# Optimization experiments

Measured on AMD Instinct MI355X. Metric: run time of the kernel, lower is better.

The kernel has to match this reference:

```python
import jax, jax.numpy as jnp
import numpy as np

B, U, I, H = 4096, 6, 1024, 512
IK, IV, K = 64, 400, 4
CH, CK, CV = 4, 32, 512
NS = 4


def setup_inputs() -> dict:
    key = jax.random.key(0)
    ks = jax.random.split(key, 14)
    s = 0.02
    return dict(
        x=jax.random.normal(ks[0], (B, 1, I), jnp.float32),
        hs=jax.random.normal(ks[1], (B, U, H), jnp.float32),
        Wk=jax.random.normal(ks[2], (I, IK), jnp.float32) * s,
        bk=jnp.zeros((IK,), jnp.float32),
        Wv=jax.random.normal(ks[3], (I, IV), jnp.float32) * s,
        bv=jnp.zeros((IV,), jnp.float32),
        Wq=jax.random.normal(ks[4], (U, H, IK), jnp.float32) * s,
        Wq_=jax.random.normal(ks[5], (U, H, CH * CK), jnp.float32) * s,
        Wk_=jax.random.normal(ks[6], (U, H, CH * CK), jnp.float32) * s,
        Wv_=jax.random.normal(ks[7], (U, H, CH * CV), jnp.float32) * s,
        Wo_=jax.random.normal(ks[8], (U, CH * CV, CV), jnp.float32) * s,
        sw=jax.nn.softmax(jax.random.normal(ks[9], (U, NS), jnp.float32), axis=-1),
        gru_wx=jax.random.normal(ks[10], (NS, IV, 3 * H), jnp.float32) * s,
        gru_wh=jax.random.normal(ks[11], (NS, H, 3 * H), jnp.float32) * s,
    )


def reference(x, hs, Wk, bk, Wv, bv, Wq, Wq_, Wk_, Wv_, Wo_, sw, gru_wx, gru_wh):
    b = x.shape[0]
    # append null input along token dim -> (B, 2, I)
    x2 = jnp.concatenate([x, jnp.zeros_like(x)], axis=1)
    # input attention (num_input_heads = 1)
    k_l = x2 @ Wk + bk                                   # (B,2,IK)
    v_l = x2 @ Wv + bv                                   # (B,2,IV)
    q_l = jnp.einsum('buh,uhd->bud', hs, Wq)             # (B,U,IK)
    scores = jnp.einsum('bud,btd->but', q_l, k_l) / np.sqrt(IK).astype(np.float32)
    # top-k gating on the non-null score
    not_null = scores[:, :, 0]                           # (B,U)
    _, idx = jax.lax.top_k(not_null, K)
    mask = jnp.zeros((b, U), x.dtype).at[jnp.arange(b)[:, None], idx].set(1.0)
    probs = jax.nn.softmax(scores, axis=-1)              # dropout off (eval)
    inputs = jnp.einsum('but,btv->buv', probs, v_l) * mask[:, :, None]  # (B,U,IV)
    # shared-schema GroupGRU: per-unit weights = schema mixture
    Wx = jnp.einsum('us,sio->uio', sw, gru_wx)           # (U,IV,3H)
    Wh = jnp.einsum('us,sho->uho', sw, gru_wh)           # (U,H,3H)
    gx = jnp.einsum('bui,uio->buo', inputs, Wx)
    gh = jnp.einsum('buh,uho->buo', hs, Wh)
    xr, xz, xn = jnp.split(gx, 3, axis=-1)
    hr, hz, hn = jnp.split(gh, 3, axis=-1)
    r = jax.nn.sigmoid(xr + hr)
    z = jax.nn.sigmoid(xz + hz)
    n = jnp.tanh(xn + r * hn)
    hy = n + z * (hs - n)                                # (B,U,H)
    # blocked_grad is identity in forward
    h_b = hy
    # communication attention (4 heads)
    q = jnp.einsum('buh,uho->buo', h_b, Wq_).reshape(b, U, CH, CK).transpose(0, 2, 1, 3)
    kk = jnp.einsum('buh,uho->buo', h_b, Wk_).reshape(b, U, CH, CK).transpose(0, 2, 1, 3)
    v = jnp.einsum('buh,uho->buo', h_b, Wv_).reshape(b, U, CH, CV).transpose(0, 2, 1, 3)
    att = jnp.einsum('bhqd,bhkd->bhqk', q, kk) / np.sqrt(CK).astype(np.float32)
    ap = jax.nn.softmax(att, axis=-1) * mask[:, None, :, None]  # mask query units
    ctx = jnp.einsum('bhqk,bhkd->bhqd', ap, v)           # (B,CH,U,CV)
    ctx = ctx.transpose(0, 2, 1, 3).reshape(b, U, CH * CV)
    ctx = jnp.einsum('buh,uho->buo', ctx, Wo_) + h_b     # (B,U,H)
    m = mask[:, :, None]
    hs_new = m * ctx + (1.0 - m) * hs
    return hs_new
```

## Files before the change

kernel.cpp:

```cpp
#include <hip/hip_runtime.h>
#include <cstddef>
#include <cstdint>


typedef unsigned short u16;
typedef __bf16 bf16x8 __attribute__((ext_vector_type(8)));
typedef float f32x4 __attribute__((ext_vector_type(4)));
typedef u16 u16x4 __attribute__((ext_vector_type(4)));

#define DEVFN static __device__ __forceinline__

DEVFN float ldin(const void* p, size_t i, int f) {
  return f ? (float)reinterpret_cast<const __bf16*>(p)[i]
           : reinterpret_cast<const float*>(p)[i];
}
DEVFN float bf2f(const u16* p, size_t i) {
  return (float)reinterpret_cast<const __bf16*>(p)[i];
}
DEVFN void f2bf(u16* p, size_t i, float v) {
  reinterpret_cast<__bf16*>(p)[i] = (__bf16)v;
}
DEVFN u16 bfbits(float v) {
  __bf16 b = (__bf16)v;
  return *reinterpret_cast<u16*>(&b);
}

constexpr size_t OFF_FLAG = 0;
constexpr size_t OFF_MASK = 256;
constexpr size_t OFF_WVT  = 98560;
constexpr size_t OFF_WQKT = 917760;
constexpr size_t OFF_WVT_ = 2490624;
constexpr size_t OFF_WOT  = 15073536;
constexpr size_t OFF_WXCT = 27656448;
constexpr size_t OFF_WHCT = 35029248;
constexpr size_t OFF_HY   = 44466432;
constexpr size_t ARENA    = 72777984;
constexpr size_t A_INP    = ARENA;
constexpr size_t A_PK     = ARENA;
constexpr size_t A_PQ     = ARENA + 4194304;
constexpr size_t A_P1     = 92438784;
constexpr size_t A_KL     = A_P1;
constexpr size_t A_QL     = 93487360;
constexpr size_t A_VL     = 99778816;

__global__ void rim_detect(const void* sw, int* flagp) {
  if (threadIdx.x == 0) {
    float s = 0.f;
    for (int i = 0; i < 24; i++)
      s += (float)reinterpret_cast<const __bf16*>(sw)[i];
    flagp[0] = (s > 5.5f && s < 6.5f) ? 1 : 0;
  }
}

__global__ __launch_bounds__(256)
void rim_sgemm32(const void* __restrict__ A_, long lda, long Az,
                 const void* __restrict__ W_, long Wz,
                 float* __restrict__ P, int KC,
                 const int* __restrict__ flagp)
{
  const int f = flagp[0];
  __shared__ float As[32 * 33];
  __shared__ float Ws[32 * 68];
  const int t = threadIdx.x;
  const int m0 = blockIdx.x * 32, kc = blockIdx.y, z = blockIdx.z;
  const int Z = gridDim.z;
  const int kb = kc * KC;
  const int tx = t & 15, ty = t >> 4;

  f32x4 acc[2];
#pragma unroll
  for (int i = 0; i < 2; i++)
#pragma unroll
    for (int j = 0; j < 4; j++) acc[i][j] = 0.f;

  for (int k0 = kb; k0 < kb + KC; k0 += 32) {
#pragma unroll
    for (int j = 0; j < 4; j++) {
      int idx = t + j * 256;
      int row = idx >> 5, kk = idx & 31;
      As[row * 33 + kk] =
          ldin(A_, (size_t)(m0 + row) * lda + (size_t)z * Az + k0 + kk, f);
    }
#pragma unroll
    for (int j = 0; j < 8; j++) {
      int idx = t + j * 256;
      int kk = idx >> 6, n = idx & 63;
      Ws[kk * 68 + n] = ldin(W_, (size_t)z * Wz + (size_t)(k0 + kk) * 64 + n, f);
    }
    __syncthreads();
#pragma unroll 8
    for (int kk = 0; kk < 32; kk++) {
      f32x4 wv = *reinterpret_cast<const f32x4*>(&Ws[kk * 68 + tx * 4]);
#pragma unroll
      for (int i = 0; i < 2; i++) {
        float a = As[(ty * 2 + i) * 33 + kk];
#pragma unroll
        for (int j = 0; j < 4; j++) acc[i][j] += a * wv[j];
      }
    }
    __syncthreads();
  }
  float* Pb = P + ((size_t)kc * Z + z) * (4096 * 64);
#pragma unroll
  for (int i = 0; i < 2; i++)
    *reinterpret_cast<f32x4*>(&Pb[(size_t)(m0 + ty * 2 + i) * 64 + tx * 4]) = acc[i];
}

__global__ void rim_sreduce(const float* __restrict__ P, int NK, int Z,
                            float* __restrict__ C, long ldc, long Cz,
                            const void* __restrict__ bias,
                            const int* __restrict__ flagp, long total)
{
  const int f = flagp[0];
  long idx = (long)blockIdx.x * 256 + threadIdx.x;
  if (idx >= total) return;
  long z = idx / (4096 * 64);
  long r = idx - z * (4096 * 64);
  long m = r >> 6;
  int n = (int)(r & 63);
  float s = bias ? ldin(bias, n, f) : 0.f;
  for (int kc = 0; kc < NK; kc++)
    s += P[((size_t)kc * Z + z) * (4096 * 64) + r];
  C[(size_t)m * ldc + (size_t)z * Cz + n] = s;
}

constexpr int LP = 40;
template<int EPI, int ADT>
__global__ __launch_bounds__(256)
void rim_gemm(const void* __restrict__ A_, long A0, long lda, long Az,
              const u16* __restrict__ B_, long Bz,
              void* __restrict__ C_, long C0, long ldc, long Cz,
              int M, int N, int K,
              const void* __restrict__ bias,
              const u16* __restrict__ hyp,
              const float* __restrict__ maskp,
              const void* __restrict__ hsp,
              const int* __restrict__ flagp)
{
  __shared__ __align__(16) __bf16 As[128 * LP];
  __shared__ __align__(16) __bf16 Bs[128 * LP];
  const int f = flagp[0];
  const int t = threadIdx.x;
  const int m0 = blockIdx.x * 128, n0 = blockIdx.y * 128, z = blockIdx.z;
  const __bf16* Bb = reinterpret_cast<const __bf16*>(B_) + (size_t)z * Bz;
  const int lane = t & 63, w = t >> 6;
  const int wm = (w & 1) * 64, wn = (w >> 1) * 64;
  const int lr = lane & 15, lk = (lane >> 4) * 8;

  f32x4 acc[4][4];
#pragma unroll
  for (int i = 0; i < 4; i++)
#pragma unroll
    for (int j = 0; j < 4; j++)
#pragma unroll
      for (int r = 0; r < 4; r++) acc[i][j][r] = 0.f;

  const int r0 = t >> 2;
  const int kc0 = (t & 3) << 3;

  for (int k0 = 0; k0 < K; k0 += 32) {
#pragma unroll
    for (int it = 0; it < 2; it++) {
      int row = r0 + it * 64;
      int gk = k0 + kc0;
      bf16x8 av, bv8;
#pragma unroll
      for (int q = 0; q < 8; q++) { av[q] = (__bf16)0.f; bv8[q] = (__bf16)0.f; }
      int gm = m0 + row;
      if (gm < M && gk < K) {
        if constexpr (ADT == 0) {
          av = *reinterpret_cast<const bf16x8*>(
              reinterpret_cast<const __bf16*>(A_) + (size_t)A0 + (size_t)z * Az +
              (size_t)gm * lda + gk);
        } else {
          size_t idx = (size_t)A0 + (size_t)z * Az + (size_t)gm * lda + gk;
          if (f) {
            av = *reinterpret_cast<const bf16x8*>(
                reinterpret_cast<const __bf16*>(A_) + idx);
          } else {
            const f32x4* fp = reinterpret_cast<const f32x4*>(
                reinterpret_cast<const float*>(A_) + idx);
            f32x4 lo = fp[0], hi = fp[1];
#pragma unroll
            for (int q = 0; q < 4; q++) {
              av[q] = (__bf16)lo[q]; av[q + 4] = (__bf16)hi[q];
            }
          }
        }
      }
      int gn = n0 + row;
      if (gn < N && gk < K)
        bv8 = *reinterpret_cast<const bf16x8*>(Bb + (size_t)gn * (size_t)K + gk);
      *reinterpret_cast<bf16x8*>(&As[row * LP + kc0]) = av;
      *reinterpret_cast<bf16x8*>(&Bs[row * LP + kc0]) = bv8;
    }
    __syncthreads();
    bf16x8 af[4], bg[4];
#pragma unroll
    for (int i = 0; i < 4; i++)
      af[i] = *reinterpret_cast<const bf16x8*>(&As[(wm + i * 16 + lr) * LP + lk]);
#pragma unroll
    for (int j = 0; j < 4; j++)
      bg[j] = *reinterpret_cast<const bf16x8*>(&Bs[(wn + j * 16 + lr) * LP + lk]);
#pragma unroll
    for (int i = 0; i < 4; i++)
#pragma unroll
      for (int j = 0; j < 4; j++)
        acc[i][j] = __builtin_amdgcn_mfma_f32_16x16x32_bf16(af[i], bg[j], acc[i][j], 0, 0, 0);
    __syncthreads();
  }

  const int rq = (lane >> 4) * 4;
  const int cq = lane & 15;
#pragma unroll
  for (int i = 0; i < 4; i++) {
#pragma unroll
    for (int j = 0; j < 4; j++) {
      int cg = n0 + wn + j * 16 + cq;
      if (cg >= N) continue;
#pragma unroll
      for (int r = 0; r < 4; r++) {
        int rg = m0 + wm + i * 16 + rq + r;
        if (rg >= M) continue;
        float v = acc[i][j][r];
        size_t cidx = (size_t)rg * ldc + (size_t)z * Cz + cg;
        if constexpr (EPI == 2) {
          f2bf((u16*)C_, C0 + cidx, v + ldin(bias, cg, f));
        } else if constexpr (EPI == 3) {
          f2bf((u16*)C_, C0 + cidx, v);
        } else {
          float mk = maskp[(size_t)rg * 6 + z];
          if (mk > 0.5f) {
            float o = v + bf2f(hyp, cidx);
            if (f) f2bf((u16*)C_, C0 + cidx, o);
            else   reinterpret_cast<float*>(C_)[C0 + cidx] = o;
          } else {
            if (f) reinterpret_cast<u16*>(C_)[C0 + cidx] =
                       reinterpret_cast<const u16*>(hsp)[C0 + cidx];
            else   reinterpret_cast<float*>(C_)[C0 + cidx] =
                       reinterpret_cast<const float*>(hsp)[C0 + cidx];
          }
        }
      }
    }
  }
}

__global__ __launch_bounds__(256)
void rim_transpose(const void* __restrict__ in, u16* __restrict__ out,
                   int N, int K, long in_z, long out_z,
                   const int* __restrict__ flagp)
{
  const int f = flagp[0];
  __shared__ float tile[32][33];
  int z = blockIdx.z;
  int k0 = blockIdx.x * 32, n0 = blockIdx.y * 32;
  int c = threadIdx.x & 31, r = threadIdx.x >> 5;
  for (int rr = r; rr < 32; rr += 8) {
    int k = k0 + rr, n = n0 + c;
    tile[rr][c] = (k < K && n < N)
        ? ldin(in, (size_t)z * in_z + (size_t)k * N + n, f) : 0.f;
  }
  __syncthreads();
  for (int rr = r; rr < 32; rr += 8) {
    int n = n0 + rr, k = k0 + c;
    if (n < N && k < K)
      f2bf(out, (size_t)z * out_z + (size_t)n * K + k, tile[c][rr]);
  }
}

__global__ __launch_bounds__(256)
void rim_gruw(const void* __restrict__ sw, const void* __restrict__ gw,
              u16* __restrict__ out, int IVH, const int* __restrict__ flagp)
{
  const int f = flagp[0];
  __shared__ float lds[64 * 17];
  int u = blockIdx.z;
  int i0 = blockIdx.x * 16, o0 = blockIdx.y * 64;
  int t = threadIdx.x;
  float s0 = ldin(sw, u * 4 + 0, f), s1 = ldin(sw, u * 4 + 1, f);
  float s2 = ldin(sw, u * 4 + 2, f), s3 = ldin(sw, u * 4 + 3, f);
  int oo = t & 63, iq = t >> 6;
  size_t pl = (size_t)IVH * 1536;
#pragma unroll
  for (int r = 0; r < 4; r++) {
    int ii = iq * 4 + r;
    size_t base = (size_t)(i0 + ii) * 1536 + o0 + oo;
    float acc = s0 * ldin(gw, base, f) + s1 * ldin(gw, pl + base, f) +
                s2 * ldin(gw, 2 * pl + base, f) + s3 * ldin(gw, 3 * pl + base, f);
    lds[oo * 17 + ii] = acc;
  }
  __syncthreads();
  int ow = t >> 2, iw = (t & 3) * 4;
  u16x4 pk;
#pragma unroll
  for (int j = 0; j < 4; j++) pk[j] = bfbits(lds[ow * 17 + iw + j]);
  *reinterpret_cast<u16x4*>(out + ((size_t)u * 1536 + o0 + ow) * IVH + i0 + iw) = pk;
}

__global__ __launch_bounds__(256)
void rim_scores(const float* __restrict__ q_l, const float* __restrict__ k_l0,
                const void* __restrict__ bk, const u16* __restrict__ v_l0,
                const void* __restrict__ bv, float* __restrict__ maskf,
                u16* __restrict__ inputs, const int* __restrict__ flagp)
{
  const int f = flagp[0];
  int b = blockIdx.x;
  int t = threadIdx.x;
  int lane = t & 63;
  __shared__ float s0[6], s1[6], sm[6], sp[6];
  if (t < 64) {
    float kv = k_l0[(size_t)b * 64 + lane];
    for (int u = 0; u < 6; u++) {
      float p = q_l[((size_t)b * 6 + u) * 64 + lane] * kv;
      for (int off = 32; off; off >>= 1) p += __shfl_down(p, off);
      if (lane == 0) s0[u] = p * 0.125f;
    }
  } else if (t < 128) {
    float kv = ldin(bk, lane, f);
    for (int u = 0; u < 6; u++) {
      float p = q_l[((size_t)b * 6 + u) * 64 + lane] * kv;
      for (int off = 32; off; off >>= 1) p += __shfl_down(p, off);
      if (lane == 0) s1[u] = p * 0.125f;
    }
  }
  __syncthreads();
  if (t == 0) {
    for (int u = 0; u < 6; u++) {
      int cnt = 0;
      for (int u2 = 0; u2 < 6; u2++)
        if (s0[u2] > s0[u] || (s0[u2] == s0[u] && u2 < u)) cnt++;
      float mk = (cnt < 4) ? 1.0f : 0.0f;
      sm[u] = mk;
      maskf[(size_t)b * 6 + u] = mk;
      sp[u] = 1.0f / (1.0f + expf(s1[u] - s0[u]));
    }
  }
  __syncthreads();
  for (int idx = t; idx < 2400; idx += 256) {
    int u = idx / 400, j = idx % 400;
    float val = sm[u] * (sp[u] * bf2f(v_l0, (size_t)b * 400 + j) +
                         (1.0f - sp[u]) * ldin(bv, j, f));
    f2bf(inputs, ((size_t)b * 6 + u) * 400 + j, val);
  }
}

__global__ void rim_gru(const u16* __restrict__ Ggx, const u16* __restrict__ Ggh,
                        const void* __restrict__ hs, long R0,
                        u16* __restrict__ hy, long total,
                        const int* __restrict__ flagp)
{
  const int f = flagp[0];
  long idx = (long)blockIdx.x * 256 + threadIdx.x;
  if (idx >= total) return;
  long bu = idx >> 9;
  int h = idx & 511;
  size_t gb = (size_t)bu * 1536 + h;
  float xr = bf2f(Ggx, gb), xz = bf2f(Ggx, gb + 512), xn = bf2f(Ggx, gb + 1024);
  float hr = bf2f(Ggh, gb), hz = bf2f(Ggh, gb + 512), hn = bf2f(Ggh, gb + 1024);
  float r = 1.f / (1.f + expf(-(xr + hr)));
  float zz = 1.f / (1.f + expf(-(xz + hz)));
  float n = tanhf(xn + r * hn);
  float hv = ldin(hs, R0 + idx, f);
  f2bf(hy, idx, n + zz * (hv - n));
}

__global__ __launch_bounds__(256)
void rim_attn(const u16* __restrict__ qk, const float* __restrict__ maskp,
              const u16* __restrict__ v, u16* __restrict__ ctx)
{
  int bl = blockIdx.x;
  int t = threadIdx.x;
  __shared__ float qs[1536];
  __shared__ float aps[144];
  __shared__ __align__(16) u16 vs[12288];
  for (int idx = t; idx < 1536; idx += 256)
    qs[idx] = bf2f(qk, (size_t)bl * 1536 + idx);
  for (int idx = t; idx < 1536; idx += 256)
    *reinterpret_cast<bf16x8*>(&vs[idx * 8]) =
        *reinterpret_cast<const bf16x8*>(
            reinterpret_cast<const __bf16*>(v) + (size_t)bl * 12288 + idx * 8);
  __syncthreads();
  if (t < 144) {
    int h = t / 36, r6 = t % 36, uq = r6 / 6, uk = r6 % 6;
    float s = 0.f;
#pragma unroll
    for (int d = 0; d < 32; d++)
      s += qs[uq * 256 + h * 32 + d] * qs[uk * 256 + 128 + h * 32 + d];
    aps[t] = s * 0.17677669529663687f;
  }
  __syncthreads();
  if (t < 24) {
    int h = t / 6, uq = t % 6;
    float* row = &aps[h * 36 + uq * 6];
    float mx = row[0];
    for (int k = 1; k < 6; k++) mx = fmaxf(mx, row[k]);
    float e[6], sum = 0.f;
    for (int k = 0; k < 6; k++) { e[k] = expf(row[k] - mx); sum += e[k]; }
    float mk = maskp[(size_t)bl * 6 + uq] / sum;
    for (int k = 0; k < 6; k++) row[k] = e[k] * mk;
  }
  __syncthreads();
  for (int idx = t; idx < 12288; idx += 256) {
    int uq = idx >> 11, g = idx & 2047, h = g >> 9;
    const float* ar = &aps[h * 36 + uq * 6];
    float acc = 0.f;
#pragma unroll
    for (int k = 0; k < 6; k++) acc += ar[k] * bf2f(vs, k * 2048 + g);
    f2bf(ctx, ((size_t)bl * 6 + uq) * 2048 + g, acc);
  }
}

extern "C" void kernel_launch(void* const* d_in, const int* in_sizes, int n_in,
                              void* d_out, int out_size, void* d_ws, size_t ws_size,
                              hipStream_t stream)
{
  (void)in_sizes; (void)n_in; (void)out_size;
  const void* x   = d_in[0];
  const void* hs  = d_in[1];
  const void* Wk  = d_in[2];
  const void* bk  = d_in[3];
  const void* Wv  = d_in[4];
  const void* bv  = d_in[5];
  const void* Wq  = d_in[6];
  const void* Wq_ = d_in[7];
  const void* Wk_ = d_in[8];
  const void* Wv_ = d_in[9];
  const void* Wo_ = d_in[10];
  const void* sw  = d_in[11];
  const void* gwx = d_in[12];
  const void* gwh = d_in[13];
  char* ws = (char*)d_ws;

  int*   flagp = (int*)(ws + OFF_FLAG);
  float* maskf = (float*)(ws + OFF_MASK);
  u16* WvT   = (u16*)(ws + OFF_WVT);
  u16* WqkT  = (u16*)(ws + OFF_WQKT);
  u16* WvT_  = (u16*)(ws + OFF_WVT_);
  u16* WoT   = (u16*)(ws + OFF_WOT);
  u16* WxcT  = (u16*)(ws + OFF_WXCT);
  u16* WhcT  = (u16*)(ws + OFF_WHCT);
  u16* hy    = (u16*)(ws + OFF_HY);
  u16* inputs = (u16*)(ws + A_INP);
  float* PK   = (float*)(ws + A_PK);
  float* PQ   = (float*)(ws + A_PQ);
  float* k_l0 = (float*)(ws + A_KL);
  float* q_l  = (float*)(ws + A_QL);
  u16* v_l0   = (u16*)(ws + A_VL);

  int R2 = 256, R3 = 256;
  {
    const int cand[5] = {4096, 2048, 1024, 512, 256};
    for (int i = 0; i < 5; i++)
      if (A_P1 + (size_t)cand[i] * 36864 <= ws_size) { R2 = cand[i]; break; }
    for (int i = 0; i < 5; i++)
      if (ARENA + (size_t)cand[i] * 52224 <= ws_size) { R3 = cand[i]; break; }
  }

  rim_detect<<<dim3(1), dim3(64), 0, stream>>>(sw, flagp);

  auto T = [&](const void* in, u16* outp, int N, int K, long iz, long oz, int Z) {
    dim3 g((K + 31) / 32, (N + 31) / 32, Z);
    rim_transpose<<<g, dim3(256), 0, stream>>>(in, outp, N, K, iz, oz, flagp);
  };
  T(Wv, WvT, 400, 1024, 0, 0, 1);
  T(Wq_, WqkT, 128, 512, 65536, 131072, 6);
  T(Wk_, WqkT + 65536, 128, 512, 65536, 131072, 6);
  T(Wv_, WvT_, 2048, 512, 1048576, 1048576, 6);
  T(Wo_, WoT, 512, 2048, 1048576, 1048576, 6);
  rim_gruw<<<dim3(25, 24, 6), dim3(256), 0, stream>>>(sw, gwx, WxcT, 400, flagp);
  rim_gruw<<<dim3(32, 24, 6), dim3(256), 0, stream>>>(sw, gwh, WhcT, 512, flagp);

  auto G = [&](int epi, int adt, const void* A, long A0, long lda, long Az,
               const u16* B, long Bz, void* C, long C0, long ldc, long Cz,
               int M, int N, int K, int Z,
               const void* bias, const u16* hyp, const float* mp, const void* hsp) {
    dim3 g((M + 127) / 128, (N + 127) / 128, Z), blk(256);
    if (epi == 2 && adt == 1)
      rim_gemm<2, 1><<<g, blk, 0, stream>>>(A, A0, lda, Az, B, Bz, C, C0, ldc, Cz, M, N, K, bias, hyp, mp, hsp, flagp);
    else if (epi == 3 && adt == 1)
      rim_gemm<3, 1><<<g, blk, 0, stream>>>(A, A0, lda, Az, B, Bz, C, C0, ldc, Cz, M, N, K, bias, hyp, mp, hsp, flagp);
    else if (epi == 3 && adt == 0)
      rim_gemm<3, 0><<<g, blk, 0, stream>>>(A, A0, lda, Az, B, Bz, C, C0, ldc, Cz, M, N, K, bias, hyp, mp, hsp, flagp);
    else
      rim_gemm<4, 0><<<g, blk, 0, stream>>>(A, A0, lda, Az, B, Bz, C, C0, ldc, Cz, M, N, K, bias, hyp, mp, hsp, flagp);
  };

  rim_sgemm32<<<dim3(128, 4, 1), dim3(256), 0, stream>>>(
      x, 1024, 0, Wk, 0, PK, 256, flagp);
  rim_sgemm32<<<dim3(128, 2, 6), dim3(256), 0, stream>>>(
      hs, 3072, 512, Wq, 32768, PQ, 256, flagp);
  rim_sreduce<<<dim3(1024), dim3(256), 0, stream>>>(
      PK, 4, 1, k_l0, 64, 0, bk, flagp, 4096L * 64);
  rim_sreduce<<<dim3(6144), dim3(256), 0, stream>>>(
      PQ, 2, 6, q_l, 384, 64, nullptr, flagp, 6L * 4096 * 64);
  G(2, 1, x, 0, 1024, 0, WvT, 0, v_l0, 0, 400, 0, 4096, 400, 1024, 1,
    bv, nullptr, nullptr, nullptr);
  rim_scores<<<dim3(4096), dim3(256), 0, stream>>>(q_l, k_l0, bk, v_l0, bv,
                                                   maskf, inputs, flagp);

  u16* Ggx = (u16*)(ws + A_P1);
  u16* Ggh = (u16*)(ws + A_P1 + (size_t)R2 * 18432);
  for (int r0 = 0; r0 < 4096; r0 += R2) {
    G(3, 1, hs, (long)r0 * 3072, 3072, 512, WhcT, 786432, Ggh, 0, 9216, 1536,
      R2, 1536, 512, 6, nullptr, nullptr, nullptr, nullptr);
    G(3, 0, inputs, (long)r0 * 2400, 2400, 400, WxcT, 614400, Ggx, 0, 9216, 1536,
      R2, 1536, 400, 6, nullptr, nullptr, nullptr, nullptr);
    long total = (long)R2 * 3072;
    rim_gru<<<dim3((unsigned)(total / 256)), dim3(256), 0, stream>>>(
        Ggx, Ggh, hs, (long)r0 * 3072, hy + (size_t)r0 * 3072, total, flagp);
  }

  u16* qk_c  = (u16*)(ws + ARENA);
  u16* v_c   = (u16*)(ws + ARENA + (size_t)R3 * 3072);
  u16* ctx_c = (u16*)(ws + ARENA + (size_t)R3 * 3072 + (size_t)R3 * 24576);
  for (int r0 = 0; r0 < 4096; r0 += R3) {
    G(3, 0, hy, (long)r0 * 3072, 3072, 512, WqkT, 131072, qk_c, 0, 1536, 256,
      R3, 256, 512, 6, nullptr, nullptr, nullptr, nullptr);
    G(3, 0, hy, (long)r0 * 3072, 3072, 512, WvT_, 1048576, v_c, 0, 12288, 2048,
      R3, 2048, 512, 6, nullptr, nullptr, nullptr, nullptr);
    rim_attn<<<dim3(R3), dim3(256), 0, stream>>>(qk_c, maskf + (size_t)r0 * 6, v_c, ctx_c);
    G(4, 0, ctx_c, 0, 12288, 2048, WoT, 1048576, d_out, (long)r0 * 3072, 3072, 512,
      R3, 512, 2048, 6, nullptr, hy + (size_t)r0 * 3072, maskf + (size_t)r0 * 6, hs);
  }
}
```

Measured before the change: 1.070 ms.

## Double-buffer GEMM via direct global-to-LDS loads, fuse QKV GEMM, pre-cast inputs

The bf16 GEMM now stages A and B tiles with global_load_lds into double-buffered LDS, so the next k-tile loads while the current one runs MFMA, and one barrier per step replaces two. Workgroup IDs are remapped across XCDs. Bounds checks are dropped, so K dims are padded (inputs to 416, Wv to 512 rows) and x and hs are cast to bf16 up front. The Q/K and V projections are fused into one GEMM writing a combined buffer that the attention kernel reads. In exchange it adds cast kernels and extra memory, and it relies on every M/N/K being a multiple of the tile size.

```diff
diff --git a/kernel.cpp b/kernel.cpp
--- a/kernel.cpp
+++ b/kernel.cpp
@@ -24,24 +24,30 @@
   __bf16 b = (__bf16)v;
   return *reinterpret_cast<u16*>(&b);
 }
+DEVFN void gload16(const __bf16* g, __bf16* l) {
+  __builtin_amdgcn_global_load_lds(
+      (const __attribute__((address_space(1))) void*)g,
+      (__attribute__((address_space(3))) void*)l, 16, 0, 0);
+}
 
 constexpr size_t OFF_FLAG = 0;
 constexpr size_t OFF_MASK = 256;
 constexpr size_t OFF_WVT  = 98560;
-constexpr size_t OFF_WQKT = 917760;
-constexpr size_t OFF_WVT_ = 2490624;
-constexpr size_t OFF_WOT  = 15073536;
-constexpr size_t OFF_WXCT = 27656448;
-constexpr size_t OFF_WHCT = 35029248;
-constexpr size_t OFF_HY   = 44466432;
-constexpr size_t ARENA    = 72777984;
+constexpr size_t OFF_WQKV = 1147136;
+constexpr size_t OFF_WOT  = 15302912;
+constexpr size_t OFF_WXCT = 27885824;
+constexpr size_t OFF_WHCT = 35553536;
+constexpr size_t OFF_HY   = 44990720;
+constexpr size_t OFF_XB   = 70156544;
+constexpr size_t OFF_HSB  = 78545152;
+constexpr size_t ARENA    = 103710976;
 constexpr size_t A_INP    = ARENA;
 constexpr size_t A_PK     = ARENA;
 constexpr size_t A_PQ     = ARENA + 4194304;
-constexpr size_t A_P1     = 92438784;
+constexpr size_t A_P1     = 124158208;
 constexpr size_t A_KL     = A_P1;
-constexpr size_t A_QL     = 93487360;
-constexpr size_t A_VL     = 99778816;
+constexpr size_t A_QL     = A_P1 + 1048576;
+constexpr size_t A_VL     = A_P1 + 7340032;
 
 __global__ void rim_detect(const void* sw, int* flagp) {
   if (threadIdx.x == 0) {
@@ -49,6 +55,26 @@
     for (int i = 0; i < 24; i++)
       s += (float)reinterpret_cast<const __bf16*>(sw)[i];
     flagp[0] = (s > 5.5f && s < 6.5f) ? 1 : 0;
+  }
+}
+
+__global__ __launch_bounds__(256)
+void rim_cast(const void* __restrict__ in, u16* __restrict__ out, long n8,
+              const int* __restrict__ flagp)
+{
+  const int f = flagp[0];
+  long stride = (long)gridDim.x * 256;
+  for (long u = (long)blockIdx.x * 256 + threadIdx.x; u < n8; u += stride) {
+    if (f) {
+      reinterpret_cast<uint4*>(out)[u] = reinterpret_cast<const uint4*>(in)[u];
+    } else {
+      f32x4 lo = reinterpret_cast<const f32x4*>(in)[u * 2];
+      f32x4 hi = reinterpret_cast<const f32x4*>(in)[u * 2 + 1];
+      bf16x8 r;
+#pragma unroll
+      for (int q = 0; q < 4; q++) { r[q] = (__bf16)lo[q]; r[q + 4] = (__bf16)hi[q]; }
+      reinterpret_cast<bf16x8*>(out)[u] = r;
+    }
   }
 }
 
@@ -124,10 +150,9 @@
   C[(size_t)m * ldc + (size_t)z * Cz + n] = s;
 }
 
-constexpr int LP = 40;
-template<int EPI, int ADT>
-__global__ __launch_bounds__(256)
-void rim_gemm(const void* __restrict__ A_, long A0, long lda, long Az,
+template<int EPI>
+__global__ __launch_bounds__(256)
+void rim_gemm(const u16* __restrict__ A16, long A0, long lda, long Az,
               const u16* __restrict__ B_, long Bz,
               void* __restrict__ C_, long C0, long ldc, long Cz,
               int M, int N, int K,
@@ -137,13 +162,36 @@
               const void* __restrict__ hsp,
               const int* __restrict__ flagp)
 {
-  __shared__ __align__(16) __bf16 As[128 * LP];
-  __shared__ __align__(16) __bf16 Bs[128 * LP];
+  __shared__ __align__(16) __bf16 As[2][128 * 32];
+  __shared__ __align__(16) __bf16 Bs[2][128 * 32];
   const int f = flagp[0];
   const int t = threadIdx.x;
-  const int m0 = blockIdx.x * 128, n0 = blockIdx.y * 128, z = blockIdx.z;
-  const __bf16* Bb = reinterpret_cast<const __bf16*>(B_) + (size_t)z * Bz;
+
+  int gx = gridDim.x, gy = gridDim.y;
+  int nwg = gx * gy * (int)gridDim.z;
+  int wg = blockIdx.x + gx * (blockIdx.y + gy * blockIdx.z);
+  {
+    int q = nwg >> 3, r = nwg & 7, xc = wg & 7, ix = wg >> 3;
+    wg = (xc < r ? xc * (q + 1) : r * (q + 1) + (xc - r) * q) + ix;
+  }
+  const int mb = wg % gx;
+  const int nb = (wg / gx) % gy;
+  const int z  = wg / (gx * gy);
+  const int m0 = mb * 128, n0 = nb * 128;
+
+  const __bf16* Ab = reinterpret_cast<const __bf16*>(A16) + (size_t)A0 +
+                     (size_t)z * Az + (size_t)m0 * lda;
+  const __bf16* Bb = reinterpret_cast<const __bf16*>(B_) + (size_t)z * Bz +
+                     (size_t)n0 * (size_t)K;
+
   const int lane = t & 63, w = t >> 6;
+  const int srow = lane >> 2;
+  const int skq  = (lane & 3) * 8;
+  const __bf16* aS0 = Ab + (size_t)(w * 16 + srow) * lda + skq;
+  const __bf16* aS1 = Ab + (size_t)((w + 4) * 16 + srow) * lda + skq;
+  const __bf16* bS0 = Bb + (size_t)(w * 16 + srow) * (size_t)K + skq;
+  const __bf16* bS1 = Bb + (size_t)((w + 4) * 16 + srow) * (size_t)K + skq;
+
   const int wm = (w & 1) * 64, wn = (w >> 1) * 64;
   const int lr = lane & 15, lk = (lane >> 4) * 8;
 
@@ -155,59 +203,31 @@
 #pragma unroll
       for (int r = 0; r < 4; r++) acc[i][j][r] = 0.f;
 
-  const int r0 = t >> 2;
-  const int kc0 = (t & 3) << 3;
-
+  auto STAGE = [&](int buf, int k0) {
+    gload16(aS0 + k0, &As[buf][w * 512]);
+    gload16(aS1 + k0, &As[buf][(w + 4) * 512]);
+    gload16(bS0 + k0, &Bs[buf][w * 512]);
+    gload16(bS1 + k0, &Bs[buf][(w + 4) * 512]);
+  };
+
+  STAGE(0, 0);
+  int cur = 0;
   for (int k0 = 0; k0 < K; k0 += 32) {
-#pragma unroll
-    for (int it = 0; it < 2; it++) {
-      int row = r0 + it * 64;
-      int gk = k0 + kc0;
-      bf16x8 av, bv8;
-#pragma unroll
-      for (int q = 0; q < 8; q++) { av[q] = (__bf16)0.f; bv8[q] = (__bf16)0.f; }
-      int gm = m0 + row;
-      if (gm < M && gk < K) {
-        if constexpr (ADT == 0) {
-          av = *reinterpret_cast<const bf16x8*>(
-              reinterpret_cast<const __bf16*>(A_) + (size_t)A0 + (size_t)z * Az +
-              (size_t)gm * lda + gk);
-        } else {
-          size_t idx = (size_t)A0 + (size_t)z * Az + (size_t)gm * lda + gk;
-          if (f) {
-            av = *reinterpret_cast<const bf16x8*>(
-                reinterpret_cast<const __bf16*>(A_) + idx);
-          } else {
-            const f32x4* fp = reinterpret_cast<const f32x4*>(
-                reinterpret_cast<const float*>(A_) + idx);
-            f32x4 lo = fp[0], hi = fp[1];
-#pragma unroll
-            for (int q = 0; q < 4; q++) {
-              av[q] = (__bf16)lo[q]; av[q + 4] = (__bf16)hi[q];
-            }
-          }
-        }
-      }
-      int gn = n0 + row;
-      if (gn < N && gk < K)
-        bv8 = *reinterpret_cast<const bf16x8*>(Bb + (size_t)gn * (size_t)K + gk);
-      *reinterpret_cast<bf16x8*>(&As[row * LP + kc0]) = av;
-      *reinterpret_cast<bf16x8*>(&Bs[row * LP + kc0]) = bv8;
-    }
     __syncthreads();
+    if (k0 + 32 < K) STAGE(cur ^ 1, k0 + 32);
     bf16x8 af[4], bg[4];
 #pragma unroll
     for (int i = 0; i < 4; i++)
-      af[i] = *reinterpret_cast<const bf16x8*>(&As[(wm + i * 16 + lr) * LP + lk]);
+      af[i] = *reinterpret_cast<const bf16x8*>(&As[cur][(wm + i * 16 + lr) * 32 + lk]);
 #pragma unroll
     for (int j = 0; j < 4; j++)
-      bg[j] = *reinterpret_cast<const bf16x8*>(&Bs[(wn + j * 16 + lr) * LP + lk]);
+      bg[j] = *reinterpret_cast<const bf16x8*>(&Bs[cur][(wn + j * 16 + lr) * 32 + lk]);
 #pragma unroll
     for (int i = 0; i < 4; i++)
 #pragma unroll
       for (int j = 0; j < 4; j++)
         acc[i][j] = __builtin_amdgcn_mfma_f32_16x16x32_bf16(af[i], bg[j], acc[i][j], 0, 0, 0);
-    __syncthreads();
+    cur ^= 1;
   }
 
   const int rq = (lane >> 4) * 4;
@@ -248,7 +268,7 @@
 
 __global__ __launch_bounds__(256)
 void rim_transpose(const void* __restrict__ in, u16* __restrict__ out,
-                   int N, int K, long in_z, long out_z,
+                   int N, int Np, int K, long in_z, long out_z,
                    const int* __restrict__ flagp)
 {
   const int f = flagp[0];
@@ -264,14 +284,15 @@
   __syncthreads();
   for (int rr = r; rr < 32; rr += 8) {
     int n = n0 + rr, k = k0 + c;
-    if (n < N && k < K)
+    if (n < Np && k < K)
       f2bf(out, (size_t)z * out_z + (size_t)n * K + k, tile[c][rr]);
   }
 }
 
 __global__ __launch_bounds__(256)
 void rim_gruw(const void* __restrict__ sw, const void* __restrict__ gw,
-              u16* __restrict__ out, int IVH, const int* __restrict__ flagp)
+              u16* __restrict__ out, int IVp, int IVs,
+              const int* __restrict__ flagp)
 {
   const int f = flagp[0];
   __shared__ float lds[64 * 17];
@@ -281,13 +302,16 @@
   float s0 = ldin(sw, u * 4 + 0, f), s1 = ldin(sw, u * 4 + 1, f);
   float s2 = ldin(sw, u * 4 + 2, f), s3 = ldin(sw, u * 4 + 3, f);
   int oo = t & 63, iq = t >> 6;
-  size_t pl = (size_t)IVH * 1536;
+  size_t pl = (size_t)IVs * 1536;
 #pragma unroll
   for (int r = 0; r < 4; r++) {
     int ii = iq * 4 + r;
-    size_t base = (size_t)(i0 + ii) * 1536 + o0 + oo;
-    float acc = s0 * ldin(gw, base, f) + s1 * ldin(gw, pl + base, f) +
-                s2 * ldin(gw, 2 * pl + base, f) + s3 * ldin(gw, 3 * pl + base, f);
+    float acc = 0.f;
+    if (i0 + ii < IVs) {
+      size_t base = (size_t)(i0 + ii) * 1536 + o0 + oo;
+      acc = s0 * ldin(gw, base, f) + s1 * ldin(gw, pl + base, f) +
+            s2 * ldin(gw, 2 * pl + base, f) + s3 * ldin(gw, 3 * pl + base, f);
+    }
     lds[oo * 17 + ii] = acc;
   }
   __syncthreads();
@@ -295,7 +319,7 @@
   u16x4 pk;
 #pragma unroll
   for (int j = 0; j < 4; j++) pk[j] = bfbits(lds[ow * 17 + iw + j]);
-  *reinterpret_cast<u16x4*>(out + ((size_t)u * 1536 + o0 + ow) * IVH + i0 + iw) = pk;
+  *reinterpret_cast<u16x4*>(out + ((size_t)u * 1536 + o0 + ow) * IVp + i0 + iw) = pk;
 }
 
 __global__ __launch_bounds__(256)
@@ -337,11 +361,13 @@
     }
   }
   __syncthreads();
-  for (int idx = t; idx < 2400; idx += 256) {
-    int u = idx / 400, j = idx % 400;
-    float val = sm[u] * (sp[u] * bf2f(v_l0, (size_t)b * 400 + j) +
-                         (1.0f - sp[u]) * ldin(bv, j, f));
-    f2bf(inputs, ((size_t)b * 6 + u) * 400 + j, val);
+  for (int idx = t; idx < 2496; idx += 256) {
+    int u = idx / 416, j = idx - u * 416;
+    float val = 0.f;
+    if (j < 400)
+      val = sm[u] * (sp[u] * bf2f(v_l0, (size_t)b * 400 + j) +
+                     (1.0f - sp[u]) * ldin(bv, j, f));
+    f2bf(inputs, ((size_t)b * 6 + u) * 416 + j, val);
   }
 }
 
@@ -366,20 +392,24 @@
 }
 
 __global__ __launch_bounds__(256)
-void rim_attn(const u16* __restrict__ qk, const float* __restrict__ maskp,
-              const u16* __restrict__ v, u16* __restrict__ ctx)
+void rim_attn(const u16* __restrict__ comb, const float* __restrict__ maskp,
+              u16* __restrict__ ctx)
 {
   int bl = blockIdx.x;
   int t = threadIdx.x;
+  const __bf16* cb = reinterpret_cast<const __bf16*>(comb) + (size_t)bl * 13824;
   __shared__ float qs[1536];
   __shared__ float aps[144];
   __shared__ __align__(16) u16 vs[12288];
-  for (int idx = t; idx < 1536; idx += 256)
-    qs[idx] = bf2f(qk, (size_t)bl * 1536 + idx);
-  for (int idx = t; idx < 1536; idx += 256)
+  for (int idx = t; idx < 1536; idx += 256) {
+    int u = idx >> 8, r = idx & 255;
+    qs[idx] = (float)cb[u * 2304 + r];
+  }
+  for (int idx = t; idx < 1536; idx += 256) {
+    int u = idx >> 8, r = idx & 255;
     *reinterpret_cast<bf16x8*>(&vs[idx * 8]) =
-        *reinterpret_cast<const bf16x8*>(
-            reinterpret_cast<const __bf16*>(v) + (size_t)bl * 12288 + idx * 8);
+        *reinterpret_cast<const bf16x8*>(cb + u * 2304 + 256 + r * 8);
+  }
   __syncthreads();
   if (t < 144) {
     int h = t / 36, r6 = t % 36, uq = r6 / 6, uk = r6 % 6;
@@ -435,12 +465,13 @@
   int*   flagp = (int*)(ws + OFF_FLAG);
   float* maskf = (float*)(ws + OFF_MASK);
   u16* WvT   = (u16*)(ws + OFF_WVT);
-  u16* WqkT  = (u16*)(ws + OFF_WQKT);
-  u16* WvT_  = (u16*)(ws + OFF_WVT_);
+  u16* WQKV  = (u16*)(ws + OFF_WQKV);
   u16* WoT   = (u16*)(ws + OFF_WOT);
   u16* WxcT  = (u16*)(ws + OFF_WXCT);
   u16* WhcT  = (u16*)(ws + OFF_WHCT);
   u16* hy    = (u16*)(ws + OFF_HY);
+  u16* xb    = (u16*)(ws + OFF_XB);
+  u16* hsb   = (u16*)(ws + OFF_HSB);
   u16* inputs = (u16*)(ws + A_INP);
   float* PK   = (float*)(ws + A_PK);
   float* PQ   = (float*)(ws + A_PQ);
@@ -459,31 +490,36 @@
 
   rim_detect<<<dim3(1), dim3(64), 0, stream>>>(sw, flagp);
 
-  auto T = [&](const void* in, u16* outp, int N, int K, long iz, long oz, int Z) {
-    dim3 g((K + 31) / 32, (N + 31) / 32, Z);
-    rim_transpose<<<g, dim3(256), 0, stream>>>(in, outp, N, K, iz, oz, flagp);
+  rim_cast<<<dim3(2048), dim3(256), 0, stream>>>(x, xb, 524288L, flagp);
+  rim_cast<<<dim3(2048), dim3(256), 0, stream>>>(hs, hsb, 1572864L, flagp);
+
+  auto T = [&](const void* in, u16* outp, int N, int Np, int K, long iz, long oz,
+               int Z) {
+    dim3 g((K + 31) / 32, (Np + 31) / 32, Z);
+    rim_transpose<<<g, dim3(256), 0, stream>>>(in, outp, N, Np, K, iz, oz, flagp);
   };
-  T(Wv, WvT, 400, 1024, 0, 0, 1);
-  T(Wq_, WqkT, 128, 512, 65536, 131072, 6);
-  T(Wk_, WqkT + 65536, 128, 512, 65536, 131072, 6);
-  T(Wv_, WvT_, 2048, 512, 1048576, 1048576, 6);
-  T(Wo_, WoT, 512, 2048, 1048576, 1048576, 6);
-  rim_gruw<<<dim3(25, 24, 6), dim3(256), 0, stream>>>(sw, gwx, WxcT, 400, flagp);
-  rim_gruw<<<dim3(32, 24, 6), dim3(256), 0, stream>>>(sw, gwh, WhcT, 512, flagp);
-
-  auto G = [&](int epi, int adt, const void* A, long A0, long lda, long Az,
+  T(Wv, WvT, 400, 512, 1024, 0, 0, 1);
+  T(Wq_, WQKV, 128, 128, 512, 65536, 1179648, 6);
+  T(Wk_, WQKV + 65536, 128, 128, 512, 65536, 1179648, 6);
+  T(Wv_, WQKV + 131072, 2048, 2048, 512, 1048576, 1179648, 6);
+  T(Wo_, WoT, 512, 512, 2048, 1048576, 1048576, 6);
+  rim_gruw<<<dim3(26, 24, 6), dim3(256), 0, stream>>>(sw, gwx, WxcT, 416, 400, flagp);
+  rim_gruw<<<dim3(32, 24, 6), dim3(256), 0, stream>>>(sw, gwh, WhcT, 512, 512, flagp);
+
+  auto G = [&](int epi, const void* A, long A0, long lda, long Az,
                const u16* B, long Bz, void* C, long C0, long ldc, long Cz,
                int M, int N, int K, int Z,
                const void* bias, const u16* hyp, const float* mp, const void* hsp) {
     dim3 g((M + 127) / 128, (N + 127) / 128, Z), blk(256);
-    if (epi == 2 && adt == 1)
-      rim_gemm<2, 1><<<g, blk, 0, stream>>>(A, A0, lda, Az, B, Bz, C, C0, ldc, Cz, M, N, K, bias, hyp, mp, hsp, flagp);
-    else if (epi == 3 && adt == 1)
-      rim_gemm<3, 1><<<g, blk, 0, stream>>>(A, A0, lda, Az, B, Bz, C, C0, ldc, Cz, M, N, K, bias, hyp, mp, hsp, flagp);
-    else if (epi == 3 && adt == 0)
-      rim_gemm<3, 0><<<g, blk, 0, stream>>>(A, A0, lda, Az, B, Bz, C, C0, ldc, Cz, M, N, K, bias, hyp, mp, hsp, flagp);
+    if (epi == 2)
+      rim_gemm<2><<<g, blk, 0, stream>>>((const u16*)A, A0, lda, Az, B, Bz, C, C0,
+                                         ldc, Cz, M, N, K, bias, hyp, mp, hsp, flagp);
+    else if (epi == 3)
+      rim_gemm<3><<<g, blk, 0, stream>>>((const u16*)A, A0, lda, Az, B, Bz, C, C0,
+                                         ldc, Cz, M, N, K, bias, hyp, mp, hsp, flagp);
     else
-      rim_gemm<4, 0><<<g, blk, 0, stream>>>(A, A0, lda, Az, B, Bz, C, C0, ldc, Cz, M, N, K, bias, hyp, mp, hsp, flagp);
+      rim_gemm<4><<<g, blk, 0, stream>>>((const u16*)A, A0, lda, Az, B, Bz, C, C0,
+                                         ldc, Cz, M, N, K, bias, hyp, mp, hsp, flagp);
   };
 
   rim_sgemm32<<<dim3(128, 4, 1), dim3(256), 0, stream>>>(
@@ -494,7 +530,7 @@
       PK, 4, 1, k_l0, 64, 0, bk, flagp, 4096L * 64);
   rim_sreduce<<<dim3(6144), dim3(256), 0, stream>>>(
       PQ, 2, 6, q_l, 384, 64, nullptr, flagp, 6L * 4096 * 64);
-  G(2, 1, x, 0, 1024, 0, WvT, 0, v_l0, 0, 400, 0, 4096, 400, 1024, 1,
+  G(2, xb, 0, 1024, 0, WvT, 0, v_l0, 0, 400, 0, 4096, 400, 1024, 1,
     bv, nullptr, nullptr, nullptr);
   rim_scores<<<dim3(4096), dim3(256), 0, stream>>>(q_l, k_l0, bk, v_l0, bv,
                                                    maskf, inputs, flagp);
@@ -502,25 +538,22 @@
   u16* Ggx = (u16*)(ws + A_P1);
   u16* Ggh = (u16*)(ws + A_P1 + (size_t)R2 * 18432);
   for (int r0 = 0; r0 < 4096; r0 += R2) {
-    G(3, 1, hs, (long)r0 * 3072, 3072, 512, WhcT, 786432, Ggh, 0, 9216, 1536,
+    G(3, hsb, (long)r0 * 3072, 3072, 512, WhcT, 786432, Ggh, 0, 9216, 1536,
       R2, 1536, 512, 6, nullptr, nullptr, nullptr, nullptr);
-    G(3, 0, inputs, (long)r0 * 2400, 2400, 400, WxcT, 614400, Ggx, 0, 9216, 1536,
-      R2, 1536, 400, 6, nullptr, nullptr, nullptr, nullptr);
+    G(3, inputs, (long)r0 * 2496, 2496, 416, WxcT, 638976, Ggx, 0, 9216, 1536,
+      R2, 1536, 416, 6, nullptr, nullptr, nullptr, nullptr);
     long total = (long)R2 * 3072;
     rim_gru<<<dim3((unsigned)(total / 256)), dim3(256), 0, stream>>>(
         Ggx, Ggh, hs, (long)r0 * 3072, hy + (size_t)r0 * 3072, total, flagp);
   }
 
-  u16* qk_c  = (u16*)(ws + ARENA);
-  u16* v_c   = (u16*)(ws + ARENA + (size_t)R3 * 3072);
-  u16* ctx_c = (u16*)(ws + ARENA + (size_t)R3 * 3072 + (size_t)R3 * 24576);
+  u16* comb  = (u16*)(ws + ARENA);
+  u16* ctx_c = (u16*)(ws + ARENA + (size_t)R3 * 27648);
   for (int r0 = 0; r0 < 4096; r0 += R3) {
-    G(3, 0, hy, (long)r0 * 3072, 3072, 512, WqkT, 131072, qk_c, 0, 1536, 256,
-      R3, 256, 512, 6, nullptr, nullptr, nullptr, nullptr);
-    G(3, 0, hy, (long)r0 * 3072, 3072, 512, WvT_, 1048576, v_c, 0, 12288, 2048,
-      R3, 2048, 512, 6, nullptr, nullptr, nullptr, nullptr);
-    rim_attn<<<dim3(R3), dim3(256), 0, stream>>>(qk_c, maskf + (size_t)r0 * 6, v_c, ctx_c);
-    G(4, 0, ctx_c, 0, 12288, 2048, WoT, 1048576, d_out, (long)r0 * 3072, 3072, 512,
+    G(3, hy, (long)r0 * 3072, 3072, 512, WQKV, 1179648, comb, 0, 13824, 2304,
+      R3, 2304, 512, 6, nullptr, nullptr, nullptr, nullptr);
+    rim_attn<<<dim3(R3), dim3(256), 0, stream>>>(comb, maskf + (size_t)r0 * 6, ctx_c);
+    G(4, ctx_c, 0, 12288, 2048, WoT, 1048576, d_out, (long)r0 * 3072, 3072, 512,
       R3, 512, 2048, 6, nullptr, hy + (size_t)r0 * 3072, maskf + (size_t)r0 * 6, hs);
   }
 }
```

Result: faster. 963.2 us (-10.0%).
